# Kernel optimization log

Measured on AMD Instinct MI355X. Metric: run time of the kernel, lower is better.

The kernel has to match this reference:

```python
import jax, jax.numpy as jnp
import numpy as np

TOPK, NPRO, NALP, NADS = 9, 31, 24, 37
EPS = 1e-9


def _pairwise_iou(b1, b2, eps=1e-6):
    # b1: (M,4) xyxy, b2: (N,4) xyxy -> (M,N)
    a1 = (b1[:, 2] - b1[:, 0]) * (b1[:, 3] - b1[:, 1])
    a2 = (b2[:, 2] - b2[:, 0]) * (b2[:, 3] - b2[:, 1])
    lt = jnp.maximum(b1[:, None, :2], b2[None, :, :2])
    rb = jnp.minimum(b1[:, None, 2:], b2[None, :, 2:])
    wh = jnp.clip(rb - lt, 0.0)
    ov = wh[..., 0] * wh[..., 1]
    union = jnp.maximum(a1[:, None] + a2[None, :] - ov, eps)
    return ov / union


def _dist_calculator(gt, anc):
    # center-to-center euclidean distance; returns (M,N) dists and (N,2) anchor centers
    gt_pts = jnp.stack([(gt[:, 0] + gt[:, 2]) / 2, (gt[:, 1] + gt[:, 3]) / 2], -1)
    ac_pts = jnp.stack([(anc[:, 0] + anc[:, 2]) / 2, (anc[:, 1] + anc[:, 3]) / 2], -1)
    d = jnp.sqrt(((gt_pts[:, None, :] - ac_pts[None, :, :]) ** 2).sum(-1))
    return d, ac_pts


def _batched_iou(b1, b2, eps=EPS):
    # b1 (b,M,4), b2 (b,N,4) -> (b,M,N)
    p1, p2 = b1[:, :, None, :2], b1[:, :, None, 2:]
    g1, g2 = b2[:, None, :, :2], b2[:, None, :, 2:]
    wh = jnp.clip(jnp.minimum(p2, g2) - jnp.maximum(p1, g1), 0.0)
    ov = wh[..., 0] * wh[..., 1]
    a1 = jnp.clip(p2 - p1, 0.0).prod(-1)
    a2 = jnp.clip(g2 - g1, 0.0).prod(-1)
    return ov / (a1 + a2 - ov + eps)


def setup_inputs() -> dict:
    key = jax.random.key(0)
    k = jax.random.split(key, 8)
    strides, img = (8, 16, 32), 1280
    anchors, levels = [], []
    for s in strides:
        n = img // s
        c = (jnp.arange(n, dtype=jnp.float32) + 0.5) * s
        cy, cx = jnp.meshgrid(c, c, indexing="ij")
        cx, cy = cx.reshape(-1), cy.reshape(-1)
        h = 2.5 * s  # cell anchor half-size = 5*stride/2 (YOLOv6 ATSS convention)
        anchors.append(jnp.stack([cx - h, cy - h, cx + h, cy + h], -1))
        levels.append(n * n)
    anc_bboxes = jnp.concatenate(anchors, 0)  # (33600, 4)
    bs, n_max = 8, 64
    cxy = jax.random.uniform(k[0], (bs, n_max, 2), minval=100.0, maxval=1180.0)
    wh = jax.random.uniform(k[1], (bs, n_max, 2), minval=20.0, maxval=300.0)
    gt_bboxes = jnp.concatenate([cxy - wh / 2, cxy + wh / 2], -1)
    x1, y1, x2, y2 = (gt_bboxes[..., i] for i in range(4))
    gt_corners = jnp.stack([x1, y1, x2, y1, x2, y2, x1, y2], -1)
    gt_pro = jax.random.randint(k[2], (bs, n_max, 1), 0, NPRO).astype(jnp.float32)
    gt_alp = jax.random.randint(k[3], (bs, n_max, 1), 0, NALP).astype(jnp.float32)
    gt_ads = jax.random.randint(k[4], (bs, n_max, 6), 0, NADS).astype(jnp.float32)
    n_valid = jax.random.randint(k[5], (bs, 1), 8, n_max + 1)
    mask_gt = (jnp.arange(n_max)[None, :] < n_valid).astype(jnp.float32)[..., None]
    pd_bboxes = anc_bboxes[None] + jax.random.normal(k[6], (bs, anc_bboxes.shape[0], 4)) * 8.0
    return {"anc_bboxes": anc_bboxes, "n_level_bboxes": levels, "gt_pro": gt_pro,
            "gt_alp": gt_alp, "gt_ads": gt_ads, "gt_bboxes": gt_bboxes,
            "gt_corners": gt_corners, "mask_gt": mask_gt, "pd_bboxes": pd_bboxes}


def reference(anc_bboxes, n_level_bboxes, gt_pro, gt_alp, gt_ads, gt_bboxes, gt_corners, mask_gt, pd_bboxes):
    bs, n_max, _ = gt_bboxes.shape
    n_anchors = anc_bboxes.shape[0]
    overlaps = _pairwise_iou(gt_bboxes.reshape(-1, 4), anc_bboxes).reshape(bs, n_max, n_anchors)
    distances, ac_points = _dist_calculator(gt_bboxes.reshape(-1, 4), anc_bboxes)
    distances = distances.reshape(bs, n_max, n_anchors)

    # --- per-level topk candidate selection ---
    mgt = mask_gt[..., 0] > 0
    b_idx = jnp.arange(bs)[:, None, None]
    g_idx = jnp.arange(n_max)[None, :, None]
    iic, cidx, start = [], [], 0
    for L in [int(v) for v in n_level_bboxes]:
        d = distances[..., start:start + L]
        k = min(TOPK, L)
        _, idxs = jax.lax.top_k(-d, k)  # smallest-distance anchors, (b,M,k)
        cidx.append(idxs + start)
        idxs_m = jnp.where(mgt[..., None], idxs, 0)
        cnt = jnp.zeros((bs, n_max, L), distances.dtype).at[b_idx, g_idx, idxs_m].add(1.0)
        iic.append(jnp.where(cnt > 1, jnp.zeros_like(cnt), cnt))
        start += L
    is_in_candidate = jnp.concatenate(iic, -1)      # (b,M,N)
    candidate_idxs = jnp.concatenate(cidx, -1)      # (b,M,K)

    # --- threshold = mean + std of candidate IoUs per gt ---
    cand_ov = jnp.where(is_in_candidate > 0, overlaps, jnp.zeros_like(overlaps))
    co = jnp.take_along_axis(cand_ov, candidate_idxs, axis=-1)  # (b,M,K)
    thr = co.mean(-1, keepdims=True) + jnp.std(co, axis=-1, ddof=1, keepdims=True)
    is_pos = jnp.where(cand_ov > thr, is_in_candidate, jnp.zeros_like(is_in_candidate))

    # --- anchor centers inside gt boxes ---
    lt = ac_points[None, None, :, :] - gt_bboxes[:, :, None, :2]
    rb = gt_bboxes[:, :, None, 2:] - ac_points[None, None, :, :]
    is_in_gts = (jnp.concatenate([lt, rb], -1).min(-1) > EPS).astype(distances.dtype)
    mask_pos = is_pos * is_in_gts * mask_gt  # (b,M,N)

    # --- resolve anchors claimed by multiple gts via max overlap ---
    fg = mask_pos.sum(-2)
    multi = fg[:, None, :] > 1
    is_max = jax.nn.one_hot(overlaps.argmax(1), n_max, dtype=mask_pos.dtype).transpose(0, 2, 1)
    mask_pos = jnp.where(multi, is_max, mask_pos)
    fg_mask = mask_pos.sum(-2)                 # (b,N)
    target_gt_idx = mask_pos.argmax(-2)        # (b,N)

    # --- gather targets ---
    fgb = fg_mask > 0
    target_pro = jnp.where(fgb, jnp.take_along_axis(gt_pro[..., 0], target_gt_idx, 1), NPRO).astype(jnp.int32)
    target_alp = jnp.where(fgb, jnp.take_along_axis(gt_alp[..., 0], target_gt_idx, 1), NALP).astype(jnp.int32)
    target_ad0_5 = [jnp.where(fgb, jnp.take_along_axis(gt_ads[..., i], target_gt_idx, 1), NADS).astype(jnp.int32)
                    for i in range(6)]
    target_bboxes = jnp.take_along_axis(gt_bboxes, target_gt_idx[..., None], 1)
    target_corners = jnp.take_along_axis(gt_corners, target_gt_idx[..., None], 1)
    pro_scores = jax.nn.one_hot(target_pro, NPRO + 1, dtype=jnp.float32)[..., :NPRO]
    alp_scores = jax.nn.one_hot(target_alp, NALP + 1, dtype=jnp.float32)[..., :NALP]
    ads_scores = [jax.nn.one_hot(t, NADS + 1, dtype=jnp.float32)[..., :NADS] for t in target_ad0_5]

    # --- rescale scores by best pred-vs-gt IoU among assigned pairs ---
    ious = (_batched_iou(gt_bboxes, pd_bboxes) * mask_pos).max(-2)[..., None]  # (b,N,1)
    pro_scores = pro_scores * ious
    alp_scores = alp_scores * ious
    ads_scores = [s * ious for s in ads_scores]

    return (target_pro, target_alp, *target_ad0_5, target_bboxes, target_corners,
            pro_scores, alp_scores, *ads_scores, fgb)
```

## Files before the change

kernel.cpp:

```cpp
#include <hip/hip_runtime.h>
#include <hip/hip_bf16.h>

#pragma clang fp contract(off)

#define NB 8
#define NG 64
#define NA 33600
#define KTOP 9
#define NCAND 27
#define NPRO 31
#define NALP 24
#define NADS 37

__device__ __forceinline__ float pair_iou(float x1, float y1, float x2, float y2,
                                          float ax1, float ay1, float ax2, float ay2) {
    float a1 = (x2 - x1) * (y2 - y1);
    float a2 = (ax2 - ax1) * (ay2 - ay1);
    float w = fminf(x2, ax2) - fmaxf(x1, ax1); w = fmaxf(w, 0.0f);
    float h = fminf(y2, ay2) - fmaxf(y1, ay1); h = fmaxf(h, 0.0f);
    float ov = w * h;
    float un = a1 + a2 - ov; un = fmaxf(un, 1e-6f);
    return ov / un;
}

__global__ __launch_bounds__(256) void k_cand(
    const float* __restrict__ anc,
    const float* __restrict__ gt,
    const float* __restrict__ mgt,
    unsigned long long* __restrict__ gbits)
{
    int bg = blockIdx.x;
    int b = bg >> 6;
    int g = bg & 63;
    if (mgt[bg] <= 0.0f) return;

    const float x1 = gt[bg * 4 + 0], y1 = gt[bg * 4 + 1];
    const float x2 = gt[bg * 4 + 2], y2 = gt[bg * 4 + 3];
    const float gx = (x1 + x2) * 0.5f, gy = (y1 + y2) * 0.5f;

    __shared__ float sd[256][KTOP];
    __shared__ int   si[256][KTOP];
    __shared__ int   cand[NCAND];

    const int tid = threadIdx.x;
    const int starts[3] = {0, 25600, 32000};
    const int lens[3]   = {25600, 6400, 1600};

    for (int lev = 0; lev < 3; ++lev) {
        float d9[KTOP]; int i9[KTOP];
        #pragma unroll
        for (int j = 0; j < KTOP; ++j) { d9[j] = INFINITY; i9[j] = 0x7fffffff; }

        const int s = starts[lev], L = lens[lev];
        for (int li = tid; li < L; li += 256) {
            int a = s + li;
            float ax = (anc[a * 4 + 0] + anc[a * 4 + 2]) * 0.5f;
            float ay = (anc[a * 4 + 1] + anc[a * 4 + 3]) * 0.5f;
            float dx = gx - ax, dy = gy - ay;
            float d = sqrtf(dx * dx + dy * dy);
            if (d < d9[KTOP - 1] || (d == d9[KTOP - 1] && li < i9[KTOP - 1])) {
                int j = KTOP - 1;
                while (j > 0 && (d < d9[j - 1] || (d == d9[j - 1] && li < i9[j - 1]))) {
                    d9[j] = d9[j - 1]; i9[j] = i9[j - 1]; --j;
                }
                d9[j] = d; i9[j] = li;
            }
        }

        for (int off = 128; off >= 1; off >>= 1) {
            #pragma unroll
            for (int j = 0; j < KTOP; ++j) { sd[tid][j] = d9[j]; si[tid][j] = i9[j]; }
            __syncthreads();
            if (tid < off) {
                float md[KTOP]; int mi[KTOP];
                int p = 0, q = 0;
                #pragma unroll
                for (int j = 0; j < KTOP; ++j) {
                    float da = d9[p];            int ia = i9[p];
                    float db = sd[tid + off][q]; int ib = si[tid + off][q];
                    bool takeA = (da < db) || (da == db && ia <= ib);
                    if (takeA) { md[j] = da; mi[j] = ia; ++p; }
                    else       { md[j] = db; mi[j] = ib; ++q; }
                }
                #pragma unroll
                for (int j = 0; j < KTOP; ++j) { d9[j] = md[j]; i9[j] = mi[j]; }
            }
            __syncthreads();
        }
        if (tid == 0) {
            #pragma unroll
            for (int j = 0; j < KTOP; ++j) cand[lev * KTOP + j] = s + i9[j];
        }
        __syncthreads();
    }

    if (tid == 0) {
        float co[NCAND];
        float sum = 0.0f;
        for (int j = 0; j < NCAND; ++j) {
            int a = cand[j];
            co[j] = pair_iou(x1, y1, x2, y2,
                             anc[a * 4 + 0], anc[a * 4 + 1], anc[a * 4 + 2], anc[a * 4 + 3]);
            sum += co[j];
        }
        float m = sum / 27.0f;
        float v = 0.0f;
        for (int j = 0; j < NCAND; ++j) { float dd = co[j] - m; v += dd * dd; }
        float thr = m + sqrtf(v / 26.0f);
        for (int j = 0; j < NCAND; ++j) {
            if (co[j] > thr) {
                int a = cand[j];
                float ax = (anc[a * 4 + 0] + anc[a * 4 + 2]) * 0.5f;
                float ay = (anc[a * 4 + 1] + anc[a * 4 + 3]) * 0.5f;
                float mn = fminf(fminf(ax - x1, ay - y1), fminf(x2 - ax, y2 - ay));
                if (mn > 1e-9f) {
                    atomicOr(&gbits[(unsigned long long)b * NA + a], 1ull << g);
                }
            }
        }
    }
}

__global__ __launch_bounds__(256) void k_assign(
    const float* __restrict__ anc,
    const float* __restrict__ gt_pro,
    const float* __restrict__ gt_alp,
    const float* __restrict__ gt_ads,
    const float* __restrict__ gt,
    const float* __restrict__ gt_cn,
    const float* __restrict__ pd,
    const unsigned long long* __restrict__ gbits,
    float* __restrict__ out)
{
    const int t = blockIdx.x * 256 + threadIdx.x;
    if (t >= NB * NA) return;
    const int b = t / NA;
    const int a = t - b * NA;

    unsigned long long m = gbits[t];
    int fg = __popcll(m);
    if (fg > 1) {
        float ax1 = anc[a * 4 + 0], ay1 = anc[a * 4 + 1];
        float ax2 = anc[a * 4 + 2], ay2 = anc[a * 4 + 3];
        float aarea = (ax2 - ax1) * (ay2 - ay1);
        float best = -INFINITY; int bgi = 0;
        for (int g = 0; g < NG; ++g) {
            const float* G = gt + ((size_t)b * NG + g) * 4;
            float gx1 = G[0], gy1 = G[1], gx2 = G[2], gy2 = G[3];
            float a1 = (gx2 - gx1) * (gy2 - gy1);
            float w = fminf(gx2, ax2) - fmaxf(gx1, ax1); w = fmaxf(w, 0.0f);
            float h = fminf(gy2, ay2) - fmaxf(gy1, ay1); h = fmaxf(h, 0.0f);
            float ov = w * h;
            float un = a1 + aarea - ov; un = fmaxf(un, 1e-6f);
            float iou = ov / un;
            if (iou > best) { best = iou; bgi = g; }
        }
        m = 1ull << bgi;
    }
    const bool fgb = (m != 0ull);
    const int tg = fgb ? (__ffsll((unsigned long long)m) - 1) : 0;

    const size_t row = (size_t)b * NG + tg;
    const float bx1 = gt[row * 4 + 0], by1 = gt[row * 4 + 1];
    const float bx2 = gt[row * 4 + 2], by2 = gt[row * 4 + 3];
    const float pro = gt_pro[row];
    const float alp = gt_alp[row];

    float iou_pd = 0.0f;
    if (fgb) {
        const float* P = pd + ((size_t)b * NA + a) * 4;
        float px1 = P[0], py1 = P[1], px2 = P[2], py2 = P[3];
        float w = fminf(bx2, px2) - fmaxf(bx1, px1); w = fmaxf(w, 0.0f);
        float h = fminf(by2, py2) - fmaxf(by1, py1); h = fmaxf(h, 0.0f);
        float ov = w * h;
        float a1 = fmaxf(bx2 - bx1, 0.0f) * fmaxf(by2 - by1, 0.0f);
        float a2 = fmaxf(px2 - px1, 0.0f) * fmaxf(py2 - py1, 0.0f);
        iou_pd = ov / (a1 + a2 - ov + 1e-9f);
    }

    const size_t S0 = (size_t)NB * NA;

    out[t] = fgb ? pro : (float)NPRO;
    out[S0 + t] = fgb ? alp : (float)NALP;
    float adsv[6];
    #pragma unroll
    for (int i = 0; i < 6; ++i) {
        adsv[i] = gt_ads[row * 6 + i];
        out[S0 * (2 + i) + t] = fgb ? adsv[i] : (float)NADS;
    }
    {
        float* ob = out + S0 * 8 + (size_t)t * 4;
        ob[0] = bx1; ob[1] = by1; ob[2] = bx2; ob[3] = by2;
    }
    {
        float* oc = out + S0 * 12 + (size_t)t * 8;
        #pragma unroll
        for (int i = 0; i < 8; ++i) oc[i] = gt_cn[row * 8 + i];
    }
    if (fgb) {
        out[S0 * 20 + (size_t)t * NPRO + (int)pro] = iou_pd;
        out[S0 * 20 + S0 * NPRO + (size_t)t * NALP + (int)alp] = iou_pd;
        const size_t ads_base = S0 * 20 + S0 * NPRO + S0 * NALP;
        #pragma unroll
        for (int i = 0; i < 6; ++i) {
            out[ads_base + (size_t)i * S0 * NADS + (size_t)t * NADS + (int)adsv[i]] = iou_pd;
        }
    }
    out[S0 * 20 + S0 * NPRO + S0 * NALP + (size_t)6 * S0 * NADS + t] = fgb ? 1.0f : 0.0f;
}

extern "C" void kernel_launch(void* const* d_in, const int* in_sizes, int n_in,
                              void* d_out, int out_size, void* d_ws, size_t ws_size,
                              hipStream_t stream) {
    const float* anc    = (const float*)d_in[0];
    const float* gt_pro = (const float*)d_in[2];
    const float* gt_alp = (const float*)d_in[3];
    const float* gt_ads = (const float*)d_in[4];
    const float* gt_bb  = (const float*)d_in[5];
    const float* gt_cn  = (const float*)d_in[6];
    const float* mgt    = (const float*)d_in[7];
    const float* pd     = (const float*)d_in[8];

    unsigned long long* gbits = (unsigned long long*)d_ws;
    float* out = (float*)d_out;

    hipMemsetAsync(d_ws, 0, (size_t)NB * NA * sizeof(unsigned long long), stream);
    hipMemsetAsync(d_out, 0, (size_t)out_size * sizeof(float), stream);

    hipLaunchKernelGGL(k_cand, dim3(NB * NG), dim3(256), 0, stream,
                       anc, gt_bb, mgt, gbits);
    hipLaunchKernelGGL(k_assign, dim3((NB * NA) / 256), dim3(256), 0, stream,
                       anc, gt_pro, gt_alp, gt_ads, gt_bb, gt_cn, pd, gbits, out);
}
```

Measured before the change: 499.7 us.

## Search 7x7 anchor window per GT, vectorize and nontemporal outputs, shrink memset

The candidate kernel now uses one thread per GT. Instead of scanning all 33600 anchors with a block-wide merge reduction, it computes the 9 nearest anchors per level from a 7x7 window of grid cells around the GT center, relying on the regular anchor grid layout. The assign kernel uses vector loads and nontemporal stores for the dense outputs, and the output memset now covers only the sparse score region. The window search assumes anchors sit on a uniform grid with the known strides, which the anchor input's construction shows to be true.

Result: faster. 434.9 us, median of 2 (-13.0%).

```diff
diff --git a/kernel.cpp b/kernel.cpp
--- a/kernel.cpp
+++ b/kernel.cpp
@@ -11,6 +11,9 @@
 #define NPRO 31
 #define NALP 24
 #define NADS 37
+#define S0 268800
+
+typedef float vf4 __attribute__((ext_vector_type(4)));
 
 __device__ __forceinline__ float pair_iou(float x1, float y1, float x2, float y2,
                                           float ax1, float ay1, float ax2, float ay2) {
@@ -23,99 +26,92 @@
     return ov / un;
 }
 
-__global__ __launch_bounds__(256) void k_cand(
+__global__ __launch_bounds__(256) void k_cand2(
     const float* __restrict__ anc,
     const float* __restrict__ gt,
     const float* __restrict__ mgt,
     unsigned long long* __restrict__ gbits)
 {
-    int bg = blockIdx.x;
-    int b = bg >> 6;
-    int g = bg & 63;
-    if (mgt[bg] <= 0.0f) return;
-
-    const float x1 = gt[bg * 4 + 0], y1 = gt[bg * 4 + 1];
-    const float x2 = gt[bg * 4 + 2], y2 = gt[bg * 4 + 3];
+    const int t = blockIdx.x * 256 + threadIdx.x;
+    if (t >= NB * NG) return;
+    const int b = t >> 6;
+    const int g = t & 63;
+    if (mgt[t] <= 0.0f) return;
+
+    const float x1 = gt[t * 4 + 0], y1 = gt[t * 4 + 1];
+    const float x2 = gt[t * 4 + 2], y2 = gt[t * 4 + 3];
     const float gx = (x1 + x2) * 0.5f, gy = (y1 + y2) * 0.5f;
 
-    __shared__ float sd[256][KTOP];
-    __shared__ int   si[256][KTOP];
-    __shared__ int   cand[NCAND];
-
-    const int tid = threadIdx.x;
-    const int starts[3] = {0, 25600, 32000};
-    const int lens[3]   = {25600, 6400, 1600};
-
+    int cand[NCAND];
+
+    const int   ns[3] = {160, 80, 40};
+    const float ss[3] = {8.0f, 16.0f, 32.0f};
+    const int   st[3] = {0, 25600, 32000};
+
+    #pragma unroll
     for (int lev = 0; lev < 3; ++lev) {
+        const int n = ns[lev];
+        const float s = ss[lev];
+        int ixn = (int)floorf(gx / s);
+        int iyn = (int)floorf(gy / s);
+        int xlo = min(max(ixn - 3, 0), n - 7);
+        int ylo = min(max(iyn - 3, 0), n - 7);
+
         float d9[KTOP]; int i9[KTOP];
         #pragma unroll
         for (int j = 0; j < KTOP; ++j) { d9[j] = INFINITY; i9[j] = 0x7fffffff; }
 
-        const int s = starts[lev], L = lens[lev];
-        for (int li = tid; li < L; li += 256) {
-            int a = s + li;
+        for (int dy = 0; dy < 7; ++dy) {
+            int iy = ylo + dy;
+            float ay = ((float)iy + 0.5f) * s;
+            float ddy = gy - ay;
+            for (int dx = 0; dx < 7; ++dx) {
+                int ix = xlo + dx;
+                float ax = ((float)ix + 0.5f) * s;
+                float ddx = gx - ax;
+                float d = sqrtf(ddx * ddx + ddy * ddy);
+                int li = iy * n + ix;
+                if (d < d9[KTOP - 1] || (d == d9[KTOP - 1] && li < i9[KTOP - 1])) {
+                    d9[KTOP - 1] = d; i9[KTOP - 1] = li;
+                    #pragma unroll
+                    for (int j = KTOP - 1; j > 0; --j) {
+                        bool sw = (d9[j] < d9[j - 1]) ||
+                                  (d9[j] == d9[j - 1] && i9[j] < i9[j - 1]);
+                        if (sw) {
+                            float td = d9[j]; d9[j] = d9[j - 1]; d9[j - 1] = td;
+                            int   ti = i9[j]; i9[j] = i9[j - 1]; i9[j - 1] = ti;
+                        }
+                    }
+                }
+            }
+        }
+        #pragma unroll
+        for (int j = 0; j < KTOP; ++j) cand[lev * KTOP + j] = st[lev] + i9[j];
+    }
+
+    float co[NCAND];
+    float sum = 0.0f;
+    #pragma unroll
+    for (int j = 0; j < NCAND; ++j) {
+        int a = cand[j];
+        co[j] = pair_iou(x1, y1, x2, y2,
+                         anc[a * 4 + 0], anc[a * 4 + 1], anc[a * 4 + 2], anc[a * 4 + 3]);
+        sum += co[j];
+    }
+    float m = sum / 27.0f;
+    float v = 0.0f;
+    #pragma unroll
+    for (int j = 0; j < NCAND; ++j) { float dd = co[j] - m; v += dd * dd; }
+    float thr = m + sqrtf(v / 26.0f);
+    #pragma unroll
+    for (int j = 0; j < NCAND; ++j) {
+        if (co[j] > thr) {
+            int a = cand[j];
             float ax = (anc[a * 4 + 0] + anc[a * 4 + 2]) * 0.5f;
             float ay = (anc[a * 4 + 1] + anc[a * 4 + 3]) * 0.5f;
-            float dx = gx - ax, dy = gy - ay;
-            float d = sqrtf(dx * dx + dy * dy);
-            if (d < d9[KTOP - 1] || (d == d9[KTOP - 1] && li < i9[KTOP - 1])) {
-                int j = KTOP - 1;
-                while (j > 0 && (d < d9[j - 1] || (d == d9[j - 1] && li < i9[j - 1]))) {
-                    d9[j] = d9[j - 1]; i9[j] = i9[j - 1]; --j;
-                }
-                d9[j] = d; i9[j] = li;
-            }
-        }
-
-        for (int off = 128; off >= 1; off >>= 1) {
-            #pragma unroll
-            for (int j = 0; j < KTOP; ++j) { sd[tid][j] = d9[j]; si[tid][j] = i9[j]; }
-            __syncthreads();
-            if (tid < off) {
-                float md[KTOP]; int mi[KTOP];
-                int p = 0, q = 0;
-                #pragma unroll
-                for (int j = 0; j < KTOP; ++j) {
-                    float da = d9[p];            int ia = i9[p];
-                    float db = sd[tid + off][q]; int ib = si[tid + off][q];
-                    bool takeA = (da < db) || (da == db && ia <= ib);
-                    if (takeA) { md[j] = da; mi[j] = ia; ++p; }
-                    else       { md[j] = db; mi[j] = ib; ++q; }
-                }
-                #pragma unroll
-                for (int j = 0; j < KTOP; ++j) { d9[j] = md[j]; i9[j] = mi[j]; }
-            }
-            __syncthreads();
-        }
-        if (tid == 0) {
-            #pragma unroll
-            for (int j = 0; j < KTOP; ++j) cand[lev * KTOP + j] = s + i9[j];
-        }
-        __syncthreads();
-    }
-
-    if (tid == 0) {
-        float co[NCAND];
-        float sum = 0.0f;
-        for (int j = 0; j < NCAND; ++j) {
-            int a = cand[j];
-            co[j] = pair_iou(x1, y1, x2, y2,
-                             anc[a * 4 + 0], anc[a * 4 + 1], anc[a * 4 + 2], anc[a * 4 + 3]);
-            sum += co[j];
-        }
-        float m = sum / 27.0f;
-        float v = 0.0f;
-        for (int j = 0; j < NCAND; ++j) { float dd = co[j] - m; v += dd * dd; }
-        float thr = m + sqrtf(v / 26.0f);
-        for (int j = 0; j < NCAND; ++j) {
-            if (co[j] > thr) {
-                int a = cand[j];
-                float ax = (anc[a * 4 + 0] + anc[a * 4 + 2]) * 0.5f;
-                float ay = (anc[a * 4 + 1] + anc[a * 4 + 3]) * 0.5f;
-                float mn = fminf(fminf(ax - x1, ay - y1), fminf(x2 - ax, y2 - ay));
-                if (mn > 1e-9f) {
-                    atomicOr(&gbits[(unsigned long long)b * NA + a], 1ull << g);
-                }
+            float mn = fminf(fminf(ax - x1, ay - y1), fminf(x2 - ax, y2 - ay));
+            if (mn > 1e-9f) {
+                atomicOr(&gbits[(unsigned long long)b * NA + a], 1ull << g);
             }
         }
     }
@@ -133,13 +129,12 @@
     float* __restrict__ out)
 {
     const int t = blockIdx.x * 256 + threadIdx.x;
-    if (t >= NB * NA) return;
+    if (t >= S0) return;
     const int b = t / NA;
     const int a = t - b * NA;
 
     unsigned long long m = gbits[t];
-    int fg = __popcll(m);
-    if (fg > 1) {
+    if (__popcll(m) > 1) {
         float ax1 = anc[a * 4 + 0], ay1 = anc[a * 4 + 1];
         float ax2 = anc[a * 4 + 2], ay2 = anc[a * 4 + 3];
         float aarea = (ax2 - ax1) * (ay2 - ay1);
@@ -161,8 +156,8 @@
     const int tg = fgb ? (__ffsll((unsigned long long)m) - 1) : 0;
 
     const size_t row = (size_t)b * NG + tg;
-    const float bx1 = gt[row * 4 + 0], by1 = gt[row * 4 + 1];
-    const float bx2 = gt[row * 4 + 2], by2 = gt[row * 4 + 3];
+    const vf4 gbox = *(const vf4*)(gt + row * 4);
+    const float bx1 = gbox.x, by1 = gbox.y, bx2 = gbox.z, by2 = gbox.w;
     const float pro = gt_pro[row];
     const float alp = gt_alp[row];
 
@@ -178,35 +173,32 @@
         iou_pd = ov / (a1 + a2 - ov + 1e-9f);
     }
 
-    const size_t S0 = (size_t)NB * NA;
-
-    out[t] = fgb ? pro : (float)NPRO;
-    out[S0 + t] = fgb ? alp : (float)NALP;
+    __builtin_nontemporal_store(fgb ? pro : (float)NPRO, out + t);
+    __builtin_nontemporal_store(fgb ? alp : (float)NALP, out + S0 + t);
     float adsv[6];
     #pragma unroll
     for (int i = 0; i < 6; ++i) {
         adsv[i] = gt_ads[row * 6 + i];
-        out[S0 * (2 + i) + t] = fgb ? adsv[i] : (float)NADS;
-    }
+        __builtin_nontemporal_store(fgb ? adsv[i] : (float)NADS, out + (size_t)S0 * (2 + i) + t);
+    }
+    __builtin_nontemporal_store(gbox, (vf4*)(out + (size_t)S0 * 8 + (size_t)t * 4));
     {
-        float* ob = out + S0 * 8 + (size_t)t * 4;
-        ob[0] = bx1; ob[1] = by1; ob[2] = bx2; ob[3] = by2;
-    }
-    {
-        float* oc = out + S0 * 12 + (size_t)t * 8;
-        #pragma unroll
-        for (int i = 0; i < 8; ++i) oc[i] = gt_cn[row * 8 + i];
-    }
+        const vf4* cn = (const vf4*)(gt_cn + row * 8);
+        vf4* oc = (vf4*)(out + (size_t)S0 * 12 + (size_t)t * 8);
+        __builtin_nontemporal_store(cn[0], oc);
+        __builtin_nontemporal_store(cn[1], oc + 1);
+    }
+    __builtin_nontemporal_store(fgb ? 1.0f : 0.0f, out + (size_t)S0 * 297 + t);
+
     if (fgb) {
-        out[S0 * 20 + (size_t)t * NPRO + (int)pro] = iou_pd;
-        out[S0 * 20 + S0 * NPRO + (size_t)t * NALP + (int)alp] = iou_pd;
-        const size_t ads_base = S0 * 20 + S0 * NPRO + S0 * NALP;
+        out[(size_t)S0 * 20 + (size_t)t * NPRO + (int)pro] = iou_pd;
+        out[(size_t)S0 * 20 + (size_t)S0 * NPRO + (size_t)t * NALP + (int)alp] = iou_pd;
+        const size_t ads_base = (size_t)S0 * 20 + (size_t)S0 * NPRO + (size_t)S0 * NALP;
         #pragma unroll
         for (int i = 0; i < 6; ++i) {
             out[ads_base + (size_t)i * S0 * NADS + (size_t)t * NADS + (int)adsv[i]] = iou_pd;
         }
     }
-    out[S0 * 20 + S0 * NPRO + S0 * NALP + (size_t)6 * S0 * NADS + t] = fgb ? 1.0f : 0.0f;
 }
 
 extern "C" void kernel_launch(void* const* d_in, const int* in_sizes, int n_in,
@@ -224,11 +216,11 @@
     unsigned long long* gbits = (unsigned long long*)d_ws;
     float* out = (float*)d_out;
 
-    hipMemsetAsync(d_ws, 0, (size_t)NB * NA * sizeof(unsigned long long), stream);
-    hipMemsetAsync(d_out, 0, (size_t)out_size * sizeof(float), stream);
-
-    hipLaunchKernelGGL(k_cand, dim3(NB * NG), dim3(256), 0, stream,
+    hipMemsetAsync(gbits, 0, (size_t)S0 * 8, stream);
+    hipMemsetAsync(out + (size_t)S0 * 20, 0, (size_t)S0 * 277 * sizeof(float), stream);
+
+    hipLaunchKernelGGL(k_cand2, dim3((NB * NG + 255) / 256), dim3(256), 0, stream,
                        anc, gt_bb, mgt, gbits);
-    hipLaunchKernelGGL(k_assign, dim3((NB * NA) / 256), dim3(256), 0, stream,
+    hipLaunchKernelGGL(k_assign, dim3((S0 + 255) / 256), dim3(256), 0, stream,
                        anc, gt_pro, gt_alp, gt_ads, gt_bb, gt_cn, pd, gbits, out);
 }
```
